# Performance work log

Hardware: AMD Instinct MI355X
Metric: run time of the kernel (lower is better)

Reference implementation:

```python
import jax, jax.numpy as jnp
import numpy as np

N_NODES = 50000
N_EDGES = 800000
D = 64
N_TAPS = 3  # taps[0..3] -> 4 linear layers


def setup_inputs() -> dict:
    key = jax.random.key(0)
    k1, k2, k3, k4 = jax.random.split(key, 4)
    x = jax.random.normal(k1, (N_NODES, D), dtype=jnp.float32)
    edge_index = jax.random.randint(k2, (2, N_EDGES), 0, N_NODES, dtype=jnp.int32)
    # Glorot-ish scaled weights for the K+1 taps, bias init zeros-like but random here
    W = jax.random.normal(k3, (N_TAPS + 1, D, D), dtype=jnp.float32) / jnp.sqrt(D)
    b = jax.random.normal(k4, (N_TAPS + 1, D), dtype=jnp.float32) * 0.01
    return {"x": x, "edge_index": edge_index, "W": W, "b": b}


def reference(x, edge_index, W, b):
    # y = sum_k W_k S^k x, where S is the (sum-aggregation) graph shift:
    # out[dst] += x[src]  (PyG SimpleConv, combine_root=None, edge_attr=None)
    src, dst = edge_index[0], edge_index[1]
    # tap 0: identity shift
    y = x @ W[0].T + b[0]
    for k in range(1, N_TAPS + 1):
        # sparse graph shift: gather source features, scatter-sum to targets
        x = jax.ops.segment_sum(x[src], dst, num_segments=N_NODES)
        y = y + x @ W[k].T + b[k]
    return y
```

## Files before the change

kernel.cpp:

```cpp
#include <hip/hip_runtime.h>

#define D 64
#define NB 1024
#define NBK_MAX 64
#define BCAP 20480

typedef __attribute__((ext_vector_type(8))) short bf16x8;
typedef __attribute__((ext_vector_type(4))) float f32x4;

__device__ __forceinline__ unsigned int bf16r(float f) {
    unsigned int u = __float_as_uint(f);
    return (u + 0x7fffu + ((u >> 16) & 1u)) >> 16;
}
__device__ __forceinline__ float bflo(unsigned int u) { return __uint_as_float(u << 16); }
__device__ __forceinline__ float bfhi(unsigned int u) { return __uint_as_float(u & 0xffff0000u); }

__global__ __launch_bounds__(256) void p1_kernel(
    const float* __restrict__ x, unsigned short* __restrict__ xb, int n8,
    const float* __restrict__ W, unsigned short* __restrict__ Wb, int w8,
    const int* __restrict__ src, const int* __restrict__ dst, int n_edges,
    int* __restrict__ bcursor, int* __restrict__ bpack, int nbk,
    int cgrid, int wgrid)
{
    __shared__ int lh[NBK_MAX * 8];
    __shared__ int lbase[NBK_MAX * 8];

    int tid = threadIdx.x;
    int bi  = blockIdx.x;

    if (bi < cgrid + wgrid) {
        const float* in; unsigned short* out; int t;
        if (bi < cgrid) { in = x; out = xb; t = bi * 256 + tid; if (t >= n8) return; }
        else            { in = W; out = Wb; t = (bi - cgrid) * 256 + tid; if (t >= w8) return; }
        const float4* p = reinterpret_cast<const float4*>(in) + (size_t)t * 2;
        float4 v0 = p[0], v1 = p[1];
        uint4 o;
        o.x = bf16r(v0.x) | (bf16r(v0.y) << 16);
        o.y = bf16r(v0.z) | (bf16r(v0.w) << 16);
        o.z = bf16r(v1.x) | (bf16r(v1.y) << 16);
        o.w = bf16r(v1.z) | (bf16r(v1.w) << 16);
        reinterpret_cast<uint4*>(out)[t] = o;
        return;
    }

    for (int t = tid; t < NBK_MAX * 8; t += 256) lh[t] = 0;
    __syncthreads();

    int pb = bi - cgrid - wgrid;
    int e4 = pb * 1024 + tid * 4;
    int r  = tid & 7;

    int dv[4], sv[4], bk[4], lo[4];
    bool ok[4];
    if (e4 + 4 <= n_edges) {
        int4 dd = *reinterpret_cast<const int4*>(dst + e4);
        int4 ss = *reinterpret_cast<const int4*>(src + e4);
        dv[0] = dd.x; dv[1] = dd.y; dv[2] = dd.z; dv[3] = dd.w;
        sv[0] = ss.x; sv[1] = ss.y; sv[2] = ss.z; sv[3] = ss.w;
        ok[0] = ok[1] = ok[2] = ok[3] = true;
    } else {
        #pragma unroll
        for (int j = 0; j < 4; ++j) {
            ok[j] = (e4 + j < n_edges);
            dv[j] = ok[j] ? dst[e4 + j] : 0;
            sv[j] = ok[j] ? src[e4 + j] : 0;
        }
    }
    #pragma unroll
    for (int j = 0; j < 4; ++j) {
        bk[j] = dv[j] >> 10;
        if (ok[j]) lo[j] = atomicAdd(&lh[(bk[j] << 3) | r], 1);
    }
    __syncthreads();

    if (tid < nbk) {
        int tot = 0, pbs[8];
        #pragma unroll
        for (int rr = 0; rr < 8; ++rr) { pbs[rr] = tot; tot += lh[(tid << 3) | rr]; }
        int gb = atomicAdd(&bcursor[tid], tot);
        #pragma unroll
        for (int rr = 0; rr < 8; ++rr) lbase[(tid << 3) | rr] = gb + pbs[rr];
    }
    __syncthreads();

    #pragma unroll
    for (int j = 0; j < 4; ++j) {
        if (ok[j]) {
            int pos = lbase[(bk[j] << 3) | r] + lo[j];
            bpack[bk[j] * BCAP + pos] = sv[j] | ((dv[j] & (NB - 1)) << 20);
        }
    }
}

__global__ __launch_bounds__(1024) void p2_kernel(
    const int* __restrict__ bcursor, const int* __restrict__ bpack,
    int* __restrict__ rp, int* __restrict__ csr,
    int n_nodes, int n_edges, int nbk)
{
    __shared__ int sz[NBK_MAX];
    __shared__ int lh[NB];
    __shared__ int ls[NB];

    int tid = threadIdx.x;
    int bk  = blockIdx.x;

    if (tid < NBK_MAX) sz[tid] = (tid < nbk) ? bcursor[tid] : 0;
    lh[tid] = 0;
    __syncthreads();
    if (tid == 0) {
        int a = 0;
        for (int i = 0; i < nbk; ++i) { int c = sz[i]; sz[i] = a; a += c; }
    }
    __syncthreads();

    int cnt      = bcursor[bk];
    int csr_base = sz[bk];
    const int* bp = bpack + (size_t)bk * BCAP;

    for (int i = tid; i < cnt; i += 1024) atomicAdd(&lh[bp[i] >> 20], 1);
    __syncthreads();

    int v = lh[tid];
    ls[tid] = v;
    __syncthreads();
    for (int off = 1; off < 1024; off <<= 1) {
        int t = (tid >= off) ? ls[tid - off] : 0;
        __syncthreads();
        ls[tid] += t;
        __syncthreads();
    }
    int ex = ls[tid] - v;

    int node = bk * NB + tid;
    if (node < n_nodes) rp[node] = csr_base + ex;
    if (bk == nbk - 1 && tid == 0) rp[n_nodes] = n_edges;
    __syncthreads();

    lh[tid] = ex;
    __syncthreads();
    for (int i = tid; i < cnt; i += 1024) {
        int p = bp[i];
        int pos = atomicAdd(&lh[p >> 20], 1);
        csr[csr_base + pos] = p & 0xFFFFF;
    }
}

__global__ __launch_bounds__(256) void tap_kernel(
    const float* __restrict__ xin, const float* __restrict__ W,
    const float* __restrict__ b, float* __restrict__ y,
    int n_nodes, int first)
{
    __shared__ float Wt[D * (D + 1)];
    __shared__ float bs[D];
    __shared__ float xs[4][D];

    int tid = threadIdx.x;
    for (int t = tid; t < D * D; t += 256) {
        int j = t >> 6, i = t & 63;
        Wt[i * (D + 1) + j] = W[t];
    }
    if (tid < D) bs[tid] = b[tid];

    int rl = tid >> 6;
    int j  = tid & 63;
    int row = blockIdx.x * 4 + rl;
    if (row < n_nodes) xs[rl][j] = xin[(size_t)row * D + j];
    __syncthreads();

    if (row >= n_nodes) return;

    float acc = bs[j];
    #pragma unroll 8
    for (int i = 0; i < D; ++i)
        acc = fmaf(xs[rl][i], Wt[i * (D + 1) + j], acc);

    float* yp = y + (size_t)row * D + j;
    *yp = first ? acc : (*yp + acc);
}

__global__ __launch_bounds__(256) void mfma_tap_kernel(
    const unsigned short* __restrict__ X0, const unsigned short* __restrict__ X1,
    const unsigned short* __restrict__ X2, const unsigned short* __restrict__ X3,
    const unsigned short* __restrict__ Wb, const float* __restrict__ b,
    float* __restrict__ y, int n_tiles)
{
    int wv   = threadIdx.x >> 6;
    int lane = threadIdx.x & 63;
    int tile = blockIdx.x * 4 + wv;
    if (tile >= n_tiles) return;

    int col = lane & 15;
    int kg  = lane >> 4;

    f32x4 acc[4];
    #pragma unroll
    for (int jt = 0; jt < 4; ++jt) {
        int c = jt * 16 + col;
        float bias = b[c] + b[64 + c] + b[128 + c] + b[192 + c];
        acc[jt] = (f32x4){bias, bias, bias, bias};
    }

    const unsigned short* Xs[4] = {X0, X1, X2, X3};
    size_t arow = (size_t)(tile * 16 + col) * D + kg * 8;

    #pragma unroll
    for (int m = 0; m < 4; ++m) {
        const unsigned short* Xm = Xs[m];
        #pragma unroll
        for (int s = 0; s < 2; ++s) {
            bf16x8 a = *reinterpret_cast<const bf16x8*>(Xm + arow + s * 32);
            #pragma unroll
            for (int jt = 0; jt < 4; ++jt) {
                bf16x8 bb = *reinterpret_cast<const bf16x8*>(
                    Wb + m * 4096 + (jt * 16 + col) * D + s * 32 + kg * 8);
                acc[jt] = __builtin_amdgcn_mfma_f32_16x16x32_bf16(a, bb, acc[jt], 0, 0, 0);
            }
        }
    }

    #pragma unroll
    for (int jt = 0; jt < 4; ++jt) {
        #pragma unroll
        for (int r = 0; r < 4; ++r) {
            int row = kg * 4 + r;
            y[(size_t)(tile * 16 + row) * D + jt * 16 + col] = acc[jt][r];
        }
    }
}

__global__ __launch_bounds__(256) void pull_bf16_kernel(
    const unsigned short* __restrict__ xin, unsigned short* __restrict__ xout,
    const int* __restrict__ rp, const int* __restrict__ csr, int n_nodes)
{
    int tid  = threadIdx.x;
    int wid  = (blockIdx.x * 256 + tid) >> 6;
    int lane = tid & 63;
    int half = lane >> 5;
    int hl   = lane & 31;
    int hb   = half << 5;
    int g    = (lane >> 4) & 1;
    int cl   = lane & 15;
    int node = wid * 2 + half;

    int beg = 0, end = 0;
    if (node < n_nodes) { beg = rp[node]; end = rp[node + 1]; }
    int cnt  = end - beg;
    int cntO = __shfl_xor(cnt, 32);
    int maxcnt = cnt > cntO ? cnt : cntO;

    const uint2* xu = reinterpret_cast<const uint2*>(xin);
    float a0 = 0.f, a1 = 0.f, a2 = 0.f, a3 = 0.f;

    for (int base = 0; base < maxcnt; base += 32) {
        int t = base + hl;
        int idx = (t < cnt) ? csr[beg + t] : 0;
        #pragma unroll
        for (int ii = 0; ii < 8; ++ii) {
            int el = 2 * ii + g;
            int s = __shfl(idx, hb + el);
            if (base + el < cnt) {
                uint2 u = xu[(size_t)s * 16 + cl];
                a0 += bflo(u.x); a1 += bfhi(u.x);
                a2 += bflo(u.y); a3 += bfhi(u.y);
            }
        }
        if (maxcnt - base > 16) {
            #pragma unroll
            for (int ii = 8; ii < 16; ++ii) {
                int el = 2 * ii + g;
                int s = __shfl(idx, hb + el);
                if (base + el < cnt) {
                    uint2 u = xu[(size_t)s * 16 + cl];
                    a0 += bflo(u.x); a1 += bfhi(u.x);
                    a2 += bflo(u.y); a3 += bfhi(u.y);
                }
            }
        }
    }

    a0 += __shfl_xor(a0, 16); a1 += __shfl_xor(a1, 16);
    a2 += __shfl_xor(a2, 16); a3 += __shfl_xor(a3, 16);

    if (node < n_nodes && g == 0) {
        uint2 o;
        o.x = bf16r(a0) | (bf16r(a1) << 16);
        o.y = bf16r(a2) | (bf16r(a3) << 16);
        reinterpret_cast<uint2*>(xout)[(size_t)node * 16 + cl] = o;
    }
}

__global__ __launch_bounds__(256) void scatter_kernel(
    const float* __restrict__ xin, float* __restrict__ xout,
    const int* __restrict__ src, const int* __restrict__ dst, int n_edges)
{
    int t = blockIdx.x * blockDim.x + threadIdx.x;
    int e = t >> 4;
    if (e >= n_edges) return;
    int c = (t & 15) * 4;
    int s = src[e];
    int d = dst[e];
    const float4 v = *reinterpret_cast<const float4*>(xin + (size_t)s * D + c);
    float* o = xout + (size_t)d * D + c;
    atomicAdd(o + 0, v.x);
    atomicAdd(o + 1, v.y);
    atomicAdd(o + 2, v.z);
    atomicAdd(o + 3, v.w);
}

extern "C" void kernel_launch(void* const* d_in, const int* in_sizes, int n_in,
                              void* d_out, int out_size, void* d_ws, size_t ws_size,
                              hipStream_t stream) {
    const float* x  = (const float*)d_in[0];
    const int*   ei = (const int*)d_in[1];
    const float* W  = (const float*)d_in[2];
    const float* b  = (const float*)d_in[3];
    float* y = (float*)d_out;

    int n_nodes = in_sizes[0] / D;
    int n_edges = in_sizes[1] / 2;
    const int* src = ei;
    const int* dst = ei + n_edges;

    int nbk = (n_nodes + NB - 1) / NB;

    size_t bufElems = (size_t)n_nodes * D;
    unsigned short* xb = (unsigned short*)d_ws;
    unsigned short* Ab = xb + bufElems;
    unsigned short* Bb = Ab + bufElems;
    unsigned short* Cb = Bb + bufElems;
    unsigned short* Wb = Cb + bufElems;
    int* bcursor = (int*)(Wb + 4 * D * D);
    int* bpack   = bcursor + NBK_MAX;
    int* rp      = bpack + (size_t)nbk * BCAP;
    int* csr     = rp + n_nodes + 64;

    size_t needed = (char*)(csr + n_edges) - (char*)d_ws;

    dim3 tb(256);
    dim3 tg((n_nodes + 3) / 4);
    int n8     = (int)(bufElems / 8);
    int cgrid  = (n8 + 255) / 256;
    int w8     = 4 * D * D / 8;
    int wgrid  = (w8 + 255) / 256;
    int eb     = (n_edges + 1023) / 1024;
    int pgrid  = ((n_nodes + 1) / 2 + 3) / 4;
    int n_tiles = (n_nodes + 15) / 16;
    int mgrid  = (n_tiles + 3) / 4;

    if (needed <= ws_size && (n_nodes & 15) == 0 && nbk <= NBK_MAX) {
        hipMemsetAsync(bcursor, 0, NBK_MAX * sizeof(int), stream);
        p1_kernel<<<cgrid + wgrid + eb, tb, 0, stream>>>(
            x, xb, n8, W, Wb, w8, src, dst, n_edges, bcursor, bpack, nbk,
            cgrid, wgrid);
        p2_kernel<<<nbk, 1024, 0, stream>>>(bcursor, bpack, rp, csr,
                                            n_nodes, n_edges, nbk);

        pull_bf16_kernel<<<pgrid, tb, 0, stream>>>(xb, Ab, rp, csr, n_nodes);
        pull_bf16_kernel<<<pgrid, tb, 0, stream>>>(Ab, Bb, rp, csr, n_nodes);
        pull_bf16_kernel<<<pgrid, tb, 0, stream>>>(Bb, Cb, rp, csr, n_nodes);

        mfma_tap_kernel<<<mgrid, tb, 0, stream>>>(xb, Ab, Bb, Cb, Wb, b, y, n_tiles);
    } else {
        float* A = (float*)d_ws;
        float* B = A + bufElems;
        size_t bufBytes = bufElems * sizeof(float);
        int sgrid = (n_edges * 16 + 255) / 256;
        hipMemsetAsync(A, 0, bufBytes, stream);
        hipMemsetAsync(B, 0, bufBytes, stream);
        tap_kernel<<<tg, tb, 0, stream>>>(x, W, b, y, n_nodes, 1);
        scatter_kernel<<<sgrid, tb, 0, stream>>>(x, A, src, dst, n_edges);
        tap_kernel<<<tg, tb, 0, stream>>>(A, W + D * D, b + D, y, n_nodes, 0);
        scatter_kernel<<<sgrid, tb, 0, stream>>>(A, B, src, dst, n_edges);
        hipMemsetAsync(A, 0, bufBytes, stream);
        tap_kernel<<<tg, tb, 0, stream>>>(B, W + 2 * D * D, b + 2 * D, y, n_nodes, 0);
        scatter_kernel<<<sgrid, tb, 0, stream>>>(B, A, src, dst, n_edges);
        tap_kernel<<<tg, tb, 0, stream>>>(A, W + 3 * D * D, b + 3 * D, y, n_nodes, 0);
    }
}
```

Measured before the change: 134.0 us.

## Split bf16 feature buffers into two 32-column planes for cache-resident gathers

Feature buffers are stored as two planes of 32 bf16 columns each, and each graph shift runs as two pull kernels, one per plane. This halves the gather working set per kernel (50k×64 bytes), so each plane is more likely to stay resident in cache during the random gathers. The plane order alternates between launches so the plane just written is read next. Bucket size for the CSR build also shrinks from 1024 to 512 nodes with 512-thread blocks. In exchange there are twice as many pull launches, and each gather is a narrower 4-byte load per lane.

```diff
diff --git a/kernel.cpp b/kernel.cpp
--- a/kernel.cpp
+++ b/kernel.cpp
@@ -1,9 +1,9 @@
 #include <hip/hip_runtime.h>
 
 #define D 64
-#define NB 1024
-#define NBK_MAX 64
-#define BCAP 20480
+#define NB 512
+#define NBK_MAX 128
+#define BCAP 10240
 
 typedef __attribute__((ext_vector_type(8))) short bf16x8;
 typedef __attribute__((ext_vector_type(4))) float f32x4;
@@ -20,7 +20,7 @@
     const float* __restrict__ W, unsigned short* __restrict__ Wb, int w8,
     const int* __restrict__ src, const int* __restrict__ dst, int n_edges,
     int* __restrict__ bcursor, int* __restrict__ bpack, int nbk,
-    int cgrid, int wgrid)
+    int cgrid, int wgrid, size_t planeStride)
 {
     __shared__ int lh[NBK_MAX * 8];
     __shared__ int lbase[NBK_MAX * 8];
@@ -29,17 +29,31 @@
     int bi  = blockIdx.x;
 
     if (bi < cgrid + wgrid) {
-        const float* in; unsigned short* out; int t;
-        if (bi < cgrid) { in = x; out = xb; t = bi * 256 + tid; if (t >= n8) return; }
-        else            { in = W; out = Wb; t = (bi - cgrid) * 256 + tid; if (t >= w8) return; }
-        const float4* p = reinterpret_cast<const float4*>(in) + (size_t)t * 2;
-        float4 v0 = p[0], v1 = p[1];
-        uint4 o;
-        o.x = bf16r(v0.x) | (bf16r(v0.y) << 16);
-        o.y = bf16r(v0.z) | (bf16r(v0.w) << 16);
-        o.z = bf16r(v1.x) | (bf16r(v1.y) << 16);
-        o.w = bf16r(v1.z) | (bf16r(v1.w) << 16);
-        reinterpret_cast<uint4*>(out)[t] = o;
+        if (bi < cgrid) {
+            int t = bi * 256 + tid;
+            if (t >= n8) return;
+            const float4* p = reinterpret_cast<const float4*>(x) + (size_t)t * 2;
+            float4 v0 = p[0], v1 = p[1];
+            uint4 o;
+            o.x = bf16r(v0.x) | (bf16r(v0.y) << 16);
+            o.y = bf16r(v0.z) | (bf16r(v0.w) << 16);
+            o.z = bf16r(v1.x) | (bf16r(v1.y) << 16);
+            o.w = bf16r(v1.z) | (bf16r(v1.w) << 16);
+            int node = t >> 3, c = t & 7;
+            unsigned short* plane = xb + (size_t)(c >> 2) * planeStride;
+            *reinterpret_cast<uint4*>(plane + (size_t)node * 32 + (c & 3) * 8) = o;
+        } else {
+            int t = (bi - cgrid) * 256 + tid;
+            if (t >= w8) return;
+            const float4* p = reinterpret_cast<const float4*>(W) + (size_t)t * 2;
+            float4 v0 = p[0], v1 = p[1];
+            uint4 o;
+            o.x = bf16r(v0.x) | (bf16r(v0.y) << 16);
+            o.y = bf16r(v0.z) | (bf16r(v0.w) << 16);
+            o.z = bf16r(v1.x) | (bf16r(v1.y) << 16);
+            o.w = bf16r(v1.z) | (bf16r(v1.w) << 16);
+            reinterpret_cast<uint4*>(Wb)[t] = o;
+        }
         return;
     }
 
@@ -68,7 +82,7 @@
     }
     #pragma unroll
     for (int j = 0; j < 4; ++j) {
-        bk[j] = dv[j] >> 10;
+        bk[j] = dv[j] >> 9;
         if (ok[j]) lo[j] = atomicAdd(&lh[(bk[j] << 3) | r], 1);
     }
     __syncthreads();
@@ -92,7 +106,7 @@
     }
 }
 
-__global__ __launch_bounds__(1024) void p2_kernel(
+__global__ __launch_bounds__(512) void p2_kernel(
     const int* __restrict__ bcursor, const int* __restrict__ bpack,
     int* __restrict__ rp, int* __restrict__ csr,
     int n_nodes, int n_edges, int nbk)
@@ -104,7 +118,7 @@
     int tid = threadIdx.x;
     int bk  = blockIdx.x;
 
-    if (tid < NBK_MAX) sz[tid] = (tid < nbk) ? bcursor[tid] : 0;
+    for (int t = tid; t < NBK_MAX; t += 512) sz[t] = (t < nbk) ? bcursor[t] : 0;
     lh[tid] = 0;
     __syncthreads();
     if (tid == 0) {
@@ -117,13 +131,13 @@
     int csr_base = sz[bk];
     const int* bp = bpack + (size_t)bk * BCAP;
 
-    for (int i = tid; i < cnt; i += 1024) atomicAdd(&lh[bp[i] >> 20], 1);
+    for (int i = tid; i < cnt; i += 512) atomicAdd(&lh[bp[i] >> 20], 1);
     __syncthreads();
 
     int v = lh[tid];
     ls[tid] = v;
     __syncthreads();
-    for (int off = 1; off < 1024; off <<= 1) {
+    for (int off = 1; off < 512; off <<= 1) {
         int t = (tid >= off) ? ls[tid - off] : 0;
         __syncthreads();
         ls[tid] += t;
@@ -138,7 +152,7 @@
 
     lh[tid] = ex;
     __syncthreads();
-    for (int i = tid; i < cnt; i += 1024) {
+    for (int i = tid; i < cnt; i += 512) {
         int p = bp[i];
         int pos = atomicAdd(&lh[p >> 20], 1);
         csr[csr_base + pos] = p & 0xFFFFF;
@@ -182,7 +196,7 @@
     const unsigned short* __restrict__ X0, const unsigned short* __restrict__ X1,
     const unsigned short* __restrict__ X2, const unsigned short* __restrict__ X3,
     const unsigned short* __restrict__ Wb, const float* __restrict__ b,
-    float* __restrict__ y, int n_tiles)
+    float* __restrict__ y, int n_tiles, size_t planeStride)
 {
     int wv   = threadIdx.x >> 6;
     int lane = threadIdx.x & 63;
@@ -201,14 +215,14 @@
     }
 
     const unsigned short* Xs[4] = {X0, X1, X2, X3};
-    size_t arow = (size_t)(tile * 16 + col) * D + kg * 8;
+    size_t arow = (size_t)(tile * 16 + col) * 32 + kg * 8;
 
     #pragma unroll
     for (int m = 0; m < 4; ++m) {
         const unsigned short* Xm = Xs[m];
         #pragma unroll
         for (int s = 0; s < 2; ++s) {
-            bf16x8 a = *reinterpret_cast<const bf16x8*>(Xm + arow + s * 32);
+            bf16x8 a = *reinterpret_cast<const bf16x8*>(Xm + s * planeStride + arow);
             #pragma unroll
             for (int jt = 0; jt < 4; ++jt) {
                 bf16x8 bb = *reinterpret_cast<const bf16x8*>(
@@ -228,8 +242,8 @@
     }
 }
 
-__global__ __launch_bounds__(256) void pull_bf16_kernel(
-    const unsigned short* __restrict__ xin, unsigned short* __restrict__ xout,
+__global__ __launch_bounds__(256) void pull_plane_kernel(
+    const unsigned short* __restrict__ xinp, unsigned short* __restrict__ xoutp,
     const int* __restrict__ rp, const int* __restrict__ csr, int n_nodes)
 {
     int tid  = threadIdx.x;
@@ -248,8 +262,8 @@
     int cntO = __shfl_xor(cnt, 32);
     int maxcnt = cnt > cntO ? cnt : cntO;
 
-    const uint2* xu = reinterpret_cast<const uint2*>(xin);
-    float a0 = 0.f, a1 = 0.f, a2 = 0.f, a3 = 0.f;
+    const unsigned int* xu = reinterpret_cast<const unsigned int*>(xinp);
+    float a0 = 0.f, a1 = 0.f;
 
     for (int base = 0; base < maxcnt; base += 32) {
         int t = base + hl;
@@ -259,9 +273,8 @@
             int el = 2 * ii + g;
             int s = __shfl(idx, hb + el);
             if (base + el < cnt) {
-                uint2 u = xu[(size_t)s * 16 + cl];
-                a0 += bflo(u.x); a1 += bfhi(u.x);
-                a2 += bflo(u.y); a3 += bfhi(u.y);
+                unsigned int u = xu[(size_t)s * 16 + cl];
+                a0 += bflo(u); a1 += bfhi(u);
             }
         }
         if (maxcnt - base > 16) {
@@ -270,22 +283,18 @@
                 int el = 2 * ii + g;
                 int s = __shfl(idx, hb + el);
                 if (base + el < cnt) {
-                    uint2 u = xu[(size_t)s * 16 + cl];
-                    a0 += bflo(u.x); a1 += bfhi(u.x);
-                    a2 += bflo(u.y); a3 += bfhi(u.y);
+                    unsigned int u = xu[(size_t)s * 16 + cl];
+                    a0 += bflo(u); a1 += bfhi(u);
                 }
             }
         }
     }
 
     a0 += __shfl_xor(a0, 16); a1 += __shfl_xor(a1, 16);
-    a2 += __shfl_xor(a2, 16); a3 += __shfl_xor(a3, 16);
 
     if (node < n_nodes && g == 0) {
-        uint2 o;
-        o.x = bf16r(a0) | (bf16r(a1) << 16);
-        o.y = bf16r(a2) | (bf16r(a3) << 16);
-        reinterpret_cast<uint2*>(xout)[(size_t)node * 16 + cl] = o;
+        unsigned int o = bf16r(a0) | (bf16r(a1) << 16);
+        reinterpret_cast<unsigned int*>(xoutp)[(size_t)node * 16 + cl] = o;
     }
 }
 
@@ -324,6 +333,7 @@
     int nbk = (n_nodes + NB - 1) / NB;
 
     size_t bufElems = (size_t)n_nodes * D;
+    size_t PS = (size_t)n_nodes * 32;
     unsigned short* xb = (unsigned short*)d_ws;
     unsigned short* Ab = xb + bufElems;
     unsigned short* Bb = Ab + bufElems;
@@ -351,15 +361,19 @@
         hipMemsetAsync(bcursor, 0, NBK_MAX * sizeof(int), stream);
         p1_kernel<<<cgrid + wgrid + eb, tb, 0, stream>>>(
             x, xb, n8, W, Wb, w8, src, dst, n_edges, bcursor, bpack, nbk,
-            cgrid, wgrid);
-        p2_kernel<<<nbk, 1024, 0, stream>>>(bcursor, bpack, rp, csr,
-                                            n_nodes, n_edges, nbk);
-
-        pull_bf16_kernel<<<pgrid, tb, 0, stream>>>(xb, Ab, rp, csr, n_nodes);
-        pull_bf16_kernel<<<pgrid, tb, 0, stream>>>(Ab, Bb, rp, csr, n_nodes);
-        pull_bf16_kernel<<<pgrid, tb, 0, stream>>>(Bb, Cb, rp, csr, n_nodes);
-
-        mfma_tap_kernel<<<mgrid, tb, 0, stream>>>(xb, Ab, Bb, Cb, Wb, b, y, n_tiles);
+            cgrid, wgrid, PS);
+        p2_kernel<<<nbk, 512, 0, stream>>>(bcursor, bpack, rp, csr,
+                                           n_nodes, n_edges, nbk);
+
+        pull_plane_kernel<<<pgrid, tb, 0, stream>>>(xb,      Ab,      rp, csr, n_nodes);
+        pull_plane_kernel<<<pgrid, tb, 0, stream>>>(xb + PS, Ab + PS, rp, csr, n_nodes);
+        pull_plane_kernel<<<pgrid, tb, 0, stream>>>(Ab + PS, Bb + PS, rp, csr, n_nodes);
+        pull_plane_kernel<<<pgrid, tb, 0, stream>>>(Ab,      Bb,      rp, csr, n_nodes);
+        pull_plane_kernel<<<pgrid, tb, 0, stream>>>(Bb,      Cb,      rp, csr, n_nodes);
+        pull_plane_kernel<<<pgrid, tb, 0, stream>>>(Bb + PS, Cb + PS, rp, csr, n_nodes);
+
+        mfma_tap_kernel<<<mgrid, tb, 0, stream>>>(xb, Ab, Bb, Cb, Wb, b, y,
+                                                  n_tiles, PS);
     } else {
         float* A = (float*)d_ws;
         float* B = A + bufElems;
```

Result: slower. 169.9 us (+26.8%).
